# Optimization experiments

Measured on AMD Instinct MI355X. Metric: run time of the kernel, lower is better.

The kernel has to match this reference:

```python
import jax, jax.numpy as jnp
import numpy as np

B, T, C = 16, 1023, 2048
N_LAYER, LAYER_ID = 24, 12


def setup_inputs() -> dict:
    key = jax.random.key(0)
    k0, k1, k2, k3, k4 = jax.random.split(key, 5)
    x = jax.random.normal(k0, (B, T, C), jnp.float32)
    # decay schedule exactly as in RWKV_TimeMix.__init__ (first_sa_layer_id = 1)
    f1 = 3.0 + (LAYER_ID - 1) / (N_LAYER - 2) * (1.2 - 3.0)
    f2 = 0.65 + (LAYER_ID - 1) / (N_LAYER - 2) * (0.4 - 0.65)
    h = np.arange(C, dtype=np.float64)
    decay_speed = np.power(f2, h / (C - 1) * 7) * f1
    time_decay = jnp.asarray(np.log(decay_speed), jnp.float32)          # [C]
    time_first = jnp.full((C,), float(np.log(0.3)), jnp.float32)        # [C]
    time_mix = jnp.concatenate([jnp.zeros((C // 2,), jnp.float32),
                                jnp.ones((C - C // 2,), jnp.float32)])  # [C]
    s = 0.02
    Wk = jax.random.normal(k1, (C, C), jnp.float32) * s
    Wv = jax.random.normal(k2, (C, C), jnp.float32) * s
    Wr = jax.random.normal(k3, (C, C), jnp.float32) * s
    Wo = jax.random.normal(k4, (C, C), jnp.float32) * s
    z = jnp.zeros((B, C), jnp.float32)
    return {"x": x, "time_decay": time_decay, "time_first": time_first,
            "time_mix": time_mix, "Wk": Wk, "Wv": Wv, "Wr": Wr, "Wo": Wo,
            "xx": z, "aa": z, "bb": z, "mm": z}


def reference(x, time_decay, time_first, time_mix, Wk, Wv, Wr, Wo, xx, aa, bb, mm):
    Bn, Tn, Cn = x.shape
    # time_shift: prepend carried last-token state xx, drop last
    x_shift = jnp.concatenate([xx[:, None, :], x[:, :-1, :]], axis=1)
    xm = x * time_mix + x_shift * (1.0 - time_mix)
    k = xm @ Wk.T                       # [B, T, C]
    v = xm @ Wv.T
    r = xm @ Wr.T
    # running-max renorm to the nearest power of two: ldexp(0.5, frexp(max_t k).exponent)
    kmax = jax.lax.stop_gradient(jnp.max(k, axis=1))   # [B, C], max over time
    _, expo = jnp.frexp(kmax)
    mm_new = jnp.ldexp(jnp.float32(0.5), expo)          # [B, C]
    k = jnp.exp(k - mm_new[:, None, :])
    kv = k * v
    # TimeX kernel weights: w[c, T-1-delta] = exp(-exp(time_decay[c]) * (delta-1)) = d**(delta-1),
    # w[c, T-1] = exp(time_first[c]); so wk[t] = e_first*k[t] + sum_{u<t} d^{t-1-u} k[u] -> linear scan
    d = jnp.exp(-jnp.exp(time_decay))                   # [C] per-channel decay (= w[...,-3])
    e_first = jnp.exp(time_first)                       # [C] (w[...,-1])
    rsf = jnp.exp(mm - mm_new)                          # rescale carried state to new renorm
    k_seq = jnp.concatenate([(bb * rsf)[:, None, :], k], axis=1)    # [B, T+1, C]
    kv_seq = jnp.concatenate([(aa * rsf)[:, None, :], kv], axis=1)  # [B, T+1, C]

    def step(carry, inp):
        Sk, Skv = carry
        kt, kvt = inp
        out = (e_first * kt + Sk, e_first * kvt + Skv)
        return (d * Sk + kt, d * Skv + kvt), out

    init = (jnp.zeros((Bn, Cn), x.dtype), jnp.zeros((Bn, Cn), x.dtype))
    seq = (jnp.swapaxes(k_seq, 0, 1), jnp.swapaxes(kv_seq, 0, 1))   # [T+1, B, C]
    _, (wk_s, wkv_s) = jax.lax.scan(step, init, seq)
    wk = jnp.swapaxes(wk_s[1:], 0, 1)     # drop state slot -> [B, T, C]
    wkv = jnp.swapaxes(wkv_s[1:], 0, 1)
    rwkv = jax.nn.sigmoid(r) * jnp.nan_to_num(wkv / wk)
    return rwkv @ Wo.T
```

## Files before the change

### kernel.cpp

```cpp
#include <hip/hip_runtime.h>
#include <hip/hip_bf16.h>
#include <math.h>
#include <float.h>

#define BB 16
#define TT 1023
#define CC 2048
#define M_ROWS (BB * TT)
#define MP 16384
#define N3 (3 * CC)
#define NCH 16
#define CHL 64

typedef __attribute__((ext_vector_type(8))) short bfrag;
typedef __attribute__((ext_vector_type(4))) float f32x4;
typedef __attribute__((ext_vector_type(4))) short short4v;

__device__ __forceinline__ void async16(const void* g, void* l) {
  __builtin_amdgcn_global_load_lds((const __attribute__((address_space(1))) void*)g,
                                   (__attribute__((address_space(3))) void*)l, 16, 0, 0);
}

__device__ __forceinline__ short bfb(float f) {
  __hip_bfloat16 h = __float2bfloat16(f);
  return *reinterpret_cast<short*>(&h);
}

__global__ void cast_weights(const float* __restrict__ Wk, const float* __restrict__ Wv,
                             const float* __restrict__ Wr, const float* __restrict__ Wo,
                             __hip_bfloat16* __restrict__ W3, __hip_bfloat16* __restrict__ WoB) {
  size_t i4 = (size_t)blockIdx.x * 256 + threadIdx.x;
  size_t i = i4 * 4;
  float4 a = *(const float4*)(Wk + i);
  float4 b = *(const float4*)(Wv + i);
  float4 c = *(const float4*)(Wr + i);
  float4 d = *(const float4*)(Wo + i);
  *(short4v*)((short*)W3 + i)              = short4v{bfb(a.x), bfb(a.y), bfb(a.z), bfb(a.w)};
  *(short4v*)((short*)W3 + i + CC * CC)    = short4v{bfb(b.x), bfb(b.y), bfb(b.z), bfb(b.w)};
  *(short4v*)((short*)W3 + i + 2 * CC * CC) = short4v{bfb(c.x), bfb(c.y), bfb(c.z), bfb(c.w)};
  *(short4v*)((short*)WoB + i)             = short4v{bfb(d.x), bfb(d.y), bfb(d.z), bfb(d.w)};
}

__global__ void build_xm(const float* __restrict__ x, const float* __restrict__ xx,
                         const float* __restrict__ tmix, __hip_bfloat16* __restrict__ xm) {
  int m = blockIdx.x;
  short* orow = (short*)xm + (size_t)m * CC;
  if (m >= M_ROWS) {
    for (int c = threadIdx.x; c < CC / 4; c += 256)
      ((short4v*)orow)[c] = short4v{0, 0, 0, 0};
    return;
  }
  int b = m / TT, t = m - b * TT;
  const float* xrow = x + (size_t)m * CC;
  const float* xprev = (t == 0) ? (xx + (size_t)b * CC) : (xrow - CC);
  for (int c = threadIdx.x; c < CC / 4; c += 256) {
    float4 xv = ((const float4*)xrow)[c];
    float4 pv = ((const float4*)xprev)[c];
    float4 tm = ((const float4*)tmix)[c];
    ((short4v*)orow)[c] = short4v{
        bfb(xv.x * tm.x + pv.x * (1.0f - tm.x)),
        bfb(xv.y * tm.y + pv.y * (1.0f - tm.y)),
        bfb(xv.z * tm.z + pv.z * (1.0f - tm.z)),
        bfb(xv.w * tm.w + pv.w * (1.0f - tm.w))};
  }
}

template <int MODE>
__global__ __launch_bounds__(512, 2)
void gemm256(const short* __restrict__ A, const short* __restrict__ Bw,
             float* __restrict__ outF, __hip_bfloat16* __restrict__ outV,
             __hip_bfloat16* __restrict__ outR) {
  __shared__ short lds[65536];

  const int lane = threadIdx.x & 63, wid = threadIdx.x >> 6;
  const int wr = wid >> 2, wc = wid & 3;

  const int nx = gridDim.x;
  const int nwg = nx * gridDim.y;
  const int bid = blockIdx.y * nx + blockIdx.x;
  const int q = nwg >> 3;
  const int swz = (bid & 7) * q + (bid >> 3);
  const int mBase = (swz / nx) * 256;
  const int nBase = (swz % nx) * 256;

  const int srow = lane >> 2;
  const int scol = (((lane & 3) ^ ((lane >> 3) & 3)) * 8);
  const int stgOff = wid * 1024 + lane * 8;
  const short* aSrcBase = A  + (size_t)(mBase + wid * 32 + srow) * CC + scol;
  const short* bSrcBase = Bw + (size_t)(nBase + wid * 32 + srow) * CC + scol;

  const int ldOff = (lane & 15) * 32 + (((lane >> 4) ^ ((lane >> 1) & 3)) * 8);

  f32x4 acc[2][4][4] = {};
  bfrag bq[4];

#define RGNA(buf, kh) ((buf) * 32768 + (kh) * 8192)
#define RGNB(buf, kh) (16384 + (buf) * 32768 + (kh) * 8192)

#define STG_A(buf, kh, tk) do { \
    const short* _s = aSrcBase + ((tk) * 64 + (kh) * 32); \
    short* _d = lds + RGNA(buf, kh) + stgOff; \
    async16(_s, _d); async16(_s + (size_t)16 * CC, _d + 512); } while (0)

#define STG_B(buf, kh, tk) do { \
    const short* _s = bSrcBase + ((tk) * 64 + (kh) * 32); \
    short* _d = lds + RGNB(buf, kh) + stgOff; \
    async16(_s, _d); async16(_s + (size_t)16 * CC, _d + 512); } while (0)

#define VM(n) asm volatile("s_waitcnt vmcnt(" #n ")" ::: "memory")

#define PH(buf, kh, mh, STAGE, WAIT) do { \
    bfrag aq[4]; \
    if ((mh) == 0) { \
      _Pragma("unroll") \
      for (int n = 0; n < 4; ++n) \
        bq[n] = *(const bfrag*)(lds + RGNB(buf, kh) + (wc * 64 + n * 16) * 32 + ldOff); \
    } \
    _Pragma("unroll") \
    for (int f = 0; f < 4; ++f) \
      aq[f] = *(const bfrag*)(lds + RGNA(buf, kh) + (wr * 128 + (mh) * 64 + f * 16) * 32 + ldOff); \
    STAGE; \
    __builtin_amdgcn_s_barrier(); \
    __builtin_amdgcn_s_setprio(1); \
    _Pragma("unroll") \
    for (int f = 0; f < 4; ++f) \
      _Pragma("unroll") \
      for (int n = 0; n < 4; ++n) \
        acc[mh][f][n] = __builtin_amdgcn_mfma_f32_16x16x32_bf16(aq[f], bq[n], acc[mh][f][n], 0, 0, 0); \
    __builtin_amdgcn_s_setprio(0); \
    WAIT; \
    __builtin_amdgcn_s_barrier(); } while (0)

  STG_A(0, 0, 0); STG_B(0, 0, 0);
  STG_A(0, 1, 0); STG_B(0, 1, 0);
  STG_A(1, 0, 1); STG_B(1, 0, 1);
  VM(4);
  __builtin_amdgcn_s_barrier();

  for (int ti = 0; ti < 30; ti += 2) {
    PH(0, 0, 0, STG_A(1, 1, ti + 1), );
    PH(0, 0, 1, STG_B(1, 1, ti + 1), );
    PH(0, 1, 0, STG_A(0, 0, ti + 2), );
    PH(0, 1, 1, STG_B(0, 0, ti + 2), VM(4));
    PH(1, 0, 0, STG_A(0, 1, ti + 2), );
    PH(1, 0, 1, STG_B(0, 1, ti + 2), );
    PH(1, 1, 0, STG_A(1, 0, ti + 3), );
    PH(1, 1, 1, STG_B(1, 0, ti + 3), VM(4));
  }
  PH(0, 0, 0, STG_A(1, 1, 31), );
  PH(0, 0, 1, STG_B(1, 1, 31), );
  PH(0, 1, 0, , );
  PH(0, 1, 1, , VM(4));
  PH(1, 0, 0, , );
  PH(1, 0, 1, , VM(0));
  PH(1, 1, 0, , );
  PH(1, 1, 1, , );

#undef PH
#undef VM
#undef STG_A
#undef STG_B
#undef RGNA
#undef RGNB

#pragma unroll
  for (int mh = 0; mh < 2; ++mh)
#pragma unroll
    for (int f = 0; f < 4; ++f) {
      const int row0 = mBase + wr * 128 + mh * 64 + f * 16 + (lane >> 4) * 4;
      const int col0 = nBase + wc * 64 + (lane & 15);
#pragma unroll
      for (int n = 0; n < 4; ++n) {
        const int col = col0 + n * 16;
#pragma unroll
        for (int rr = 0; rr < 4; ++rr) {
          const int row = row0 + rr;
          if (row < M_ROWS) {
            float val = acc[mh][f][n][rr];
            if constexpr (MODE == 0) {
              outF[(size_t)row * CC + col] = val;
            } else {
              if (col < CC)          outF[(size_t)row * CC + col] = val;
              else if (col < 2 * CC) outV[(size_t)row * CC + (col - CC)] = __float2bfloat16(val);
              else                   outR[(size_t)row * CC + (col - 2 * CC)] = __float2bfloat16(val);
            }
          }
        }
      }
    }
}

__global__ __launch_bounds__(1024)
void scan_fuse2(const float* __restrict__ kraw, const __hip_bfloat16* __restrict__ v,
                const __hip_bfloat16* __restrict__ r, const float* __restrict__ aa,
                const float* __restrict__ bb, const float* __restrict__ mm,
                const float* __restrict__ tdec, const float* __restrict__ tfir,
                __hip_bfloat16* __restrict__ rwkv) {
  __shared__ float sBk[NCH][64], sBkv[NCH][64], sSk[NCH][64], sSkv[NCH][64];

  const int lane = threadIdx.x & 63, wid = threadIdx.x >> 6;
  const int c = blockIdx.x * 64 + lane;
  const int b = blockIdx.y;
  const int i = b * CC + c;

  const float dexp = expf(tdec[c]);
  const float d    = expf(-dexp);
  const float ef   = expf(tfir[c]);

  const int t0 = wid * CHL;
  const int t1 = (t0 + CHL < TT) ? t0 + CHL : TT;
  const size_t base = (size_t)b * TT * CC + c;

  if (wid < NCH - 1) {
    float Bk = 0.0f, Bkv = 0.0f;
    size_t off = base + (size_t)t0 * CC;
#pragma unroll 4
    for (int t = t0; t < t1; ++t, off += CC) {
      float kk = expf(kraw[off]);
      float kv = kk * __bfloat162float(v[off]);
      Bk = d * Bk + kk;
      Bkv = d * Bkv + kv;
    }
    sBk[wid][lane] = Bk;
    sBkv[wid][lane] = Bkv;
  }
  __syncthreads();

  if (wid == 0) {
    const float d64 = expf(-dexp * (float)CHL);
    const float sc = expf(mm[i]);
    float S = bb[i] * sc, Sv = aa[i] * sc;
#pragma unroll
    for (int j = 0; j < NCH; ++j) {
      sSk[j][lane] = S;
      sSkv[j][lane] = Sv;
      if (j < NCH - 1) {
        S = d64 * S + sBk[j][lane];
        Sv = d64 * Sv + sBkv[j][lane];
      }
    }
  }
  __syncthreads();

  float S = sSk[wid][lane], Sv = sSkv[wid][lane];
  size_t off = base + (size_t)t0 * CC;
#pragma unroll 4
  for (int t = t0; t < t1; ++t, off += CC) {
    float kk = expf(kraw[off]);
    float vv = __bfloat162float(v[off]);
    float rv = __bfloat162float(r[off]);
    float kv = kk * vv;
    float wk = ef * kk + S;
    float wkv = ef * kv + Sv;
    S = d * S + kk;
    Sv = d * Sv + kv;
    float ratio = wkv / wk;
    if (isnan(ratio)) ratio = 0.0f;
    else if (isinf(ratio)) ratio = ratio > 0.0f ? FLT_MAX : -FLT_MAX;
    float sig = 1.0f / (1.0f + expf(-rv));
    rwkv[off] = __float2bfloat16(sig * ratio);
  }
}

extern "C" void kernel_launch(void* const* d_in, const int* in_sizes, int n_in,
                              void* d_out, int out_size, void* d_ws, size_t ws_size,
                              hipStream_t stream) {
  const float* x    = (const float*)d_in[0];
  const float* tdec = (const float*)d_in[1];
  const float* tfir = (const float*)d_in[2];
  const float* tmix = (const float*)d_in[3];
  const float* Wk   = (const float*)d_in[4];
  const float* Wv   = (const float*)d_in[5];
  const float* Wr   = (const float*)d_in[6];
  const float* Wo   = (const float*)d_in[7];
  const float* xx   = (const float*)d_in[8];
  const float* aa   = (const float*)d_in[9];
  const float* bb   = (const float*)d_in[10];
  const float* mm   = (const float*)d_in[11];

  char* ws = (char*)d_ws;
  size_t o = 0;
  __hip_bfloat16* W3  = (__hip_bfloat16*)(ws + o); o += (size_t)N3 * CC * 2;
  __hip_bfloat16* WoB = (__hip_bfloat16*)(ws + o); o += (size_t)CC * CC * 2;
  __hip_bfloat16* xmB = (__hip_bfloat16*)(ws + o); o += (size_t)MP * CC * 2;
  __hip_bfloat16* vB  = (__hip_bfloat16*)(ws + o); o += (size_t)MP * CC * 2;
  __hip_bfloat16* rB  = (__hip_bfloat16*)(ws + o); o += (size_t)MP * CC * 2;

  float* kraw = (float*)d_out;
  __hip_bfloat16* rwkvB = xmB;

  cast_weights<<<CC * CC / 1024, 256, 0, stream>>>(Wk, Wv, Wr, Wo, W3, WoB);
  build_xm<<<MP, 256, 0, stream>>>(x, xx, tmix, xmB);
  gemm256<1><<<dim3(N3 / 256, MP / 256), 512, 0, stream>>>(
      (const short*)xmB, (const short*)W3, kraw, vB, rB);
  scan_fuse2<<<dim3(CC / 64, BB), 1024, 0, stream>>>(kraw, vB, rB, aa, bb, mm,
                                                     tdec, tfir, rwkvB);
  gemm256<0><<<dim3(CC / 256, MP / 256), 512, 0, stream>>>(
      (const short*)rwkvB, (const short*)WoB, (float*)d_out, nullptr, nullptr);
}
```

Baseline: 697.9 us.

## Restructure GEMM main loop into two phases per K-tile with whole-tile staging

Replaces the eight fine-grained phases per pair of K-tiles, each staging one quarter-tile, with two phases per 64-wide K-tile. The first phase loads both k-halves of B and the first half of A, issues all four async copies for the next tile, then runs 32 MFMAs. The second phase computes the second M-half and waits with vmcnt(0). This halves the number of barriers and waitcnts and gives more MFMA work between syncs. In exchange it uses more registers for the doubled fragments and shortens the prefetch lead, since the next tile must be fully loaded before the following phase.

```diff
diff --git a/kernel.cpp b/kernel.cpp
--- a/kernel.cpp
+++ b/kernel.cpp
@@ -92,7 +92,7 @@
   const int ldOff = (lane & 15) * 32 + (((lane >> 4) ^ ((lane >> 1) & 3)) * 8);
 
   f32x4 acc[2][4][4] = {};
-  bfrag bq[4];
+  bfrag bq[2][4];
 
 #define RGNA(buf, kh) ((buf) * 32768 + (kh) * 8192)
 #define RGNB(buf, kh) (16384 + (buf) * 32768 + (kh) * 8192)
@@ -107,57 +107,75 @@
     short* _d = lds + RGNB(buf, kh) + stgOff; \
     async16(_s, _d); async16(_s + (size_t)16 * CC, _d + 512); } while (0)
 
-#define VM(n) asm volatile("s_waitcnt vmcnt(" #n ")" ::: "memory")
-
-#define PH(buf, kh, mh, STAGE, WAIT) do { \
-    bfrag aq[4]; \
-    if ((mh) == 0) { \
+#define STG4(buf, tk) do { \
+    STG_A(buf, 0, tk); STG_B(buf, 0, tk); \
+    STG_A(buf, 1, tk); STG_B(buf, 1, tk); } while (0)
+
+#define VM0 asm volatile("s_waitcnt vmcnt(0)" ::: "memory")
+
+#define PHA(buf, STAGE) do { \
+    bfrag aq[2][4]; \
+    _Pragma("unroll") \
+    for (int kh = 0; kh < 2; ++kh) { \
       _Pragma("unroll") \
       for (int n = 0; n < 4; ++n) \
-        bq[n] = *(const bfrag*)(lds + RGNB(buf, kh) + (wc * 64 + n * 16) * 32 + ldOff); \
+        bq[kh][n] = *(const bfrag*)(lds + RGNB(buf, kh) + (wc * 64 + n * 16) * 32 + ldOff); \
+      _Pragma("unroll") \
+      for (int f = 0; f < 4; ++f) \
+        aq[kh][f] = *(const bfrag*)(lds + RGNA(buf, kh) + (wr * 128 + f * 16) * 32 + ldOff); \
     } \
-    _Pragma("unroll") \
-    for (int f = 0; f < 4; ++f) \
-      aq[f] = *(const bfrag*)(lds + RGNA(buf, kh) + (wr * 128 + (mh) * 64 + f * 16) * 32 + ldOff); \
     STAGE; \
     __builtin_amdgcn_s_barrier(); \
     __builtin_amdgcn_s_setprio(1); \
     _Pragma("unroll") \
-    for (int f = 0; f < 4; ++f) \
-      _Pragma("unroll") \
-      for (int n = 0; n < 4; ++n) \
-        acc[mh][f][n] = __builtin_amdgcn_mfma_f32_16x16x32_bf16(aq[f], bq[n], acc[mh][f][n], 0, 0, 0); \
+    for (int kh = 0; kh < 2; ++kh) \
+      _Pragma("unroll") \
+      for (int f = 0; f < 4; ++f) \
+        _Pragma("unroll") \
+        for (int n = 0; n < 4; ++n) \
+          acc[0][f][n] = __builtin_amdgcn_mfma_f32_16x16x32_bf16(aq[kh][f], bq[kh][n], acc[0][f][n], 0, 0, 0); \
+    __builtin_amdgcn_s_setprio(0); \
+    __builtin_amdgcn_s_barrier(); } while (0)
+
+#define PHB(buf, WAIT) do { \
+    bfrag aq[2][4]; \
+    _Pragma("unroll") \
+    for (int kh = 0; kh < 2; ++kh) \
+      _Pragma("unroll") \
+      for (int f = 0; f < 4; ++f) \
+        aq[kh][f] = *(const bfrag*)(lds + RGNA(buf, kh) + (wr * 128 + 64 + f * 16) * 32 + ldOff); \
+    __builtin_amdgcn_s_barrier(); \
+    __builtin_amdgcn_s_setprio(1); \
+    _Pragma("unroll") \
+    for (int kh = 0; kh < 2; ++kh) \
+      _Pragma("unroll") \
+      for (int f = 0; f < 4; ++f) \
+        _Pragma("unroll") \
+        for (int n = 0; n < 4; ++n) \
+          acc[1][f][n] = __builtin_amdgcn_mfma_f32_16x16x32_bf16(aq[kh][f], bq[kh][n], acc[1][f][n], 0, 0, 0); \
     __builtin_amdgcn_s_setprio(0); \
     WAIT; \
     __builtin_amdgcn_s_barrier(); } while (0)
 
-  STG_A(0, 0, 0); STG_B(0, 0, 0);
-  STG_A(0, 1, 0); STG_B(0, 1, 0);
-  STG_A(1, 0, 1); STG_B(1, 0, 1);
-  VM(4);
+  STG4(0, 0);
+  VM0;
   __builtin_amdgcn_s_barrier();
 
   for (int ti = 0; ti < 30; ti += 2) {
-    PH(0, 0, 0, STG_A(1, 1, ti + 1), );
-    PH(0, 0, 1, STG_B(1, 1, ti + 1), );
-    PH(0, 1, 0, STG_A(0, 0, ti + 2), );
-    PH(0, 1, 1, STG_B(0, 0, ti + 2), VM(4));
-    PH(1, 0, 0, STG_A(0, 1, ti + 2), );
-    PH(1, 0, 1, STG_B(0, 1, ti + 2), );
-    PH(1, 1, 0, STG_A(1, 0, ti + 3), );
-    PH(1, 1, 1, STG_B(1, 0, ti + 3), VM(4));
-  }
-  PH(0, 0, 0, STG_A(1, 1, 31), );
-  PH(0, 0, 1, STG_B(1, 1, 31), );
-  PH(0, 1, 0, , );
-  PH(0, 1, 1, , VM(4));
-  PH(1, 0, 0, , );
-  PH(1, 0, 1, , VM(0));
-  PH(1, 1, 0, , );
-  PH(1, 1, 1, , );
-
-#undef PH
-#undef VM
+    PHA(0, STG4(1, ti + 1));
+    PHB(0, VM0);
+    PHA(1, STG4(0, ti + 2));
+    PHB(1, VM0);
+  }
+  PHA(0, STG4(1, 31));
+  PHB(0, VM0);
+  PHA(1, );
+  PHB(1, );
+
+#undef PHA
+#undef PHB
+#undef VM0
+#undef STG4
 #undef STG_A
 #undef STG_B
 #undef RGNA
```

Measured after the change: 787.1 us. 1.13x slower.
